# Optimization experiments

Hardware: AMD Instinct MI355X
Metric: run time of the kernel (lower is better)

The kernel has to match this reference:

```python
import jax, jax.numpy as jnp
import numpy as np

ALPHA = 0.02
NEG = -9e15

def lrelu(x):
    return jnp.where(x >= 0, x, ALPHA * x)

def layer_norm(x, eps=1e-5):
    m = jnp.mean(x, axis=-1, keepdims=True)
    v = jnp.var(x, axis=-1, keepdims=True)
    return (x - m) * jax.lax.rsqrt(v + eps)

def setup_inputs() -> dict:
    key = jax.random.key(0)
    ks = jax.random.split(key, 10)
    B, N, F_IN, D = 8, 2048, 10, 128
    h = jax.random.normal(ks[0], (B, N, F_IN), jnp.float32)
    adj = jax.random.randint(ks[1], (B, N, N), 0, 2, jnp.int32)
    s = 0.1
    return {
        "h": h,
        "adj": adj,
        "W1": jax.random.normal(ks[2], (D, F_IN), jnp.float32) * s,
        "b1": jax.random.normal(ks[3], (D,), jnp.float32) * s,
        "Wg": jax.random.normal(ks[4], (D, D), jnp.float32) * s,
        "bg": jax.random.normal(ks[5], (D,), jnp.float32) * s,
        "a1": jax.random.normal(ks[6], (D,), jnp.float32) * s,
        "a2": jax.random.normal(ks[7], (D,), jnp.float32) * s,
        "W2": jax.random.normal(ks[8], (2, D), jnp.float32) * s,
        "b2": jax.random.normal(ks[9], (2,), jnp.float32) * s,
    }

def reference(h, adj, W1, b1, Wg, bg, a1, a2, W2, b2):
    # fc1 + layernorm + leakyrelu
    x = h @ W1.T + b1                      # [B,N,128]
    x = lrelu(layer_norm(x))
    # GAT layer
    Wh = x @ Wg.T + bg                     # [B,N,128]
    e1 = Wh @ a1                           # [B,N]
    e2 = Wh @ a2                           # [B,N]
    e = lrelu(e1[:, :, None] + e2[:, None, :])  # [B,N,N]
    e = jnp.where(adj != 0, e, NEG)
    attn = jax.nn.softmax(e, axis=2)
    hp = jnp.einsum('bij,bjd->bid', attn, Wh)    # [B,N,128]
    hp = lrelu(layer_norm(hp))
    # global max pool over nodes
    pooled = jnp.max(hp, axis=1)           # [B,128]
    out = pooled @ W2.T + b2               # [B,2]
    return jax.nn.log_softmax(out, axis=-1)
```

## Files before the change

kernel.cpp:

```cpp
#include <hip/hip_runtime.h>

#define B 8
#define N 2048
#define FIN 10
#define D 128
#define ALPHA 0.02f
#define BR 32
#define TI 32
#define JC 128

typedef short bf8 __attribute__((ext_vector_type(8)));
typedef short s4v __attribute__((ext_vector_type(4)));
typedef float f32x4 __attribute__((ext_vector_type(4)));

__device__ __forceinline__ float lrelu(float x) { return x >= 0.f ? x : ALPHA * x; }

__device__ __forceinline__ short f2b(float f) {
    unsigned u = __float_as_uint(f);
    return (short)((u + 0x7fffu + ((u >> 16) & 1u)) >> 16);
}
__device__ __forceinline__ float b2f(short s) {
    return __uint_as_float(((unsigned)(unsigned short)s) << 16);
}

__device__ __forceinline__ unsigned enc_key(float v) {
    unsigned b = __float_as_uint(v);
    return (b & 0x80000000u) ? ~b : (b | 0x80000000u);
}
__device__ __forceinline__ float dec_key(unsigned k) {
    unsigned b = (k & 0x80000000u) ? (k & 0x7fffffffu) : ~k;
    return __uint_as_float(b);
}

__global__ __launch_bounds__(256) void k_proj(
    const float* __restrict__ h, const float* __restrict__ W1, const float* __restrict__ b1,
    const float* __restrict__ Wg, const float* __restrict__ bg,
    const float* __restrict__ a1, const float* __restrict__ a2,
    unsigned short* __restrict__ WhT, float* __restrict__ e1g, float* __restrict__ e2g)
{
    __shared__ __align__(16) short xep_lds[32 * 136];
    __shared__ __align__(16) short wg_lds[D * 136];
    __shared__ float W1_lds[D * 11];
    __shared__ float h_lds[BR * FIN];
    __shared__ float ep1[2][BR], ep2[2][BR];

    const int t = threadIdx.x;
    const int r0 = blockIdx.x * BR;
    const int bb = r0 >> 11;
    const int jloc = r0 & (N - 1);

    for (int idx = t; idx < D * FIN; idx += 256)
        W1_lds[(idx / FIN) * 11 + (idx % FIN)] = W1[idx];
    for (int idx = t; idx < BR * FIN; idx += 256)
        h_lds[idx] = h[(size_t)r0 * FIN + idx];
    __syncthreads();

    {
        const int dr = t >> 4;
        const int j8 = t & 15;
        #pragma unroll
        for (int pass = 0; pass < 8; pass++) {
            int dd = pass * 16 + dr;
            float4 f0 = *(const float4*)&Wg[dd * D + j8 * 8];
            float4 f1 = *(const float4*)&Wg[dd * D + j8 * 8 + 4];
            bf8 v;
            v[0] = f2b(f0.x); v[1] = f2b(f0.y); v[2] = f2b(f0.z); v[3] = f2b(f0.w);
            v[4] = f2b(f1.x); v[5] = f2b(f1.y); v[6] = f2b(f1.z); v[7] = f2b(f1.w);
            *(bf8*)&wg_lds[dd * 136 + j8 * 8] = v;
        }
    }

    const int w = t >> 6, lane = t & 63;
    {
        float b1v0 = b1[lane], b1v1 = b1[lane + 64];
        for (int i = 0; i < 8; i++) {
            int r = w * 8 + i;
            float s0 = b1v0, s1 = b1v1;
            const float* hr = &h_lds[r * FIN];
            #pragma unroll
            for (int k = 0; k < FIN; k++) {
                float hv = hr[k];
                s0 += hv * W1_lds[lane * 11 + k];
                s1 += hv * W1_lds[(lane + 64) * 11 + k];
            }
            float sm = s0 + s1, sq = s0 * s0 + s1 * s1;
            #pragma unroll
            for (int m = 1; m <= 32; m <<= 1) { sm += __shfl_xor(sm, m); sq += __shfl_xor(sq, m); }
            float mean = sm * (1.f / D);
            float var  = sq * (1.f / D) - mean * mean;
            float rs = rsqrtf(var + 1e-5f);
            xep_lds[r * 136 + lane]      = f2b(lrelu((s0 - mean) * rs));
            xep_lds[r * 136 + lane + 64] = f2b(lrelu((s1 - mean) * rs));
        }
    }
    __syncthreads();

    const int l15 = lane & 15, q = lane >> 4;
    const int mw = w & 1, np = w >> 1;
    f32x4 acc[4];
    #pragma unroll
    for (int nt = 0; nt < 4; nt++)
        #pragma unroll
        for (int r = 0; r < 4; r++) acc[nt][r] = 0.f;

    #pragma unroll
    for (int ks = 0; ks < 4; ks++) {
        bf8 av = *(const bf8*)&xep_lds[(mw * 16 + l15) * 136 + ks * 32 + q * 8];
        #pragma unroll
        for (int nt = 0; nt < 4; nt++) {
            bf8 bv = *(const bf8*)&wg_lds[((np * 4 + nt) * 16 + l15) * 136 + ks * 32 + q * 8];
            acc[nt] = __builtin_amdgcn_mfma_f32_16x16x32_bf16(av, bv, acc[nt], 0, 0, 0);
        }
    }

    float e1p[4] = {0.f, 0.f, 0.f, 0.f}, e2p[4] = {0.f, 0.f, 0.f, 0.f};
    #pragma unroll
    for (int nt = 0; nt < 4; nt++) {
        int col = (np * 4 + nt) * 16 + l15;
        float bgv = bg[col], a1v = a1[col], a2v = a2[col];
        #pragma unroll
        for (int r = 0; r < 4; r++) {
            float v = acc[nt][r] + bgv;
            acc[nt][r] = v;
            e1p[r] += v * a1v;
            e2p[r] += v * a2v;
        }
    }
    #pragma unroll
    for (int m = 1; m <= 8; m <<= 1) {
        #pragma unroll
        for (int r = 0; r < 4; r++) { e1p[r] += __shfl_xor(e1p[r], m); e2p[r] += __shfl_xor(e2p[r], m); }
    }
    if (l15 == 0) {
        #pragma unroll
        for (int r = 0; r < 4; r++) {
            ep1[np][mw * 16 + q * 4 + r] = e1p[r];
            ep2[np][mw * 16 + q * 4 + r] = e2p[r];
        }
    }
    __syncthreads();
    if (t < BR) {
        e1g[r0 + t] = ep1[0][t] + ep1[1][t];
        e2g[r0 + t] = ep2[0][t] + ep2[1][t];
    }
    #pragma unroll
    for (int nt = 0; nt < 4; nt++) {
        int col = (np * 4 + nt) * 16 + l15;
        #pragma unroll
        for (int r = 0; r < 4; r++)
            xep_lds[col * 36 + mw * 16 + q * 4 + r] = f2b(acc[nt][r]);
    }
    __syncthreads();
    {
        const int col = t >> 1, jh = (t & 1) * 16;
        unsigned short* dst = WhT + ((size_t)(bb * D + col)) * N + jloc + jh;
        #pragma unroll
        for (int i2 = 0; i2 < 4; i2++)
            *(uint2*)(dst + i2 * 4) = *(const uint2*)&xep_lds[col * 36 + jh + i2 * 4];
    }
}

__global__ __launch_bounds__(256) void k_attn(
    const int* __restrict__ adj, const unsigned short* __restrict__ WhT,
    const float* __restrict__ e1g, const float* __restrict__ e2g,
    unsigned* __restrict__ pooled)
{
    __shared__ __align__(16) short pT[TI * 136];
    __shared__ __align__(16) short whT[D * 136];
    __shared__ float e1_lds[TI];
    __shared__ float l_lds[TI];
    __shared__ float statsp[2][TI][2];
    __shared__ float maxb[2][D];

    const int t = threadIdx.x;
    const int b = blockIdx.y;
    const int i0 = blockIdx.x * TI;

    if (t < TI) { e1_lds[t] = e1g[b * N + i0 + t]; l_lds[t] = 0.f; }

    const int w = t >> 6, lane = t & 63;
    const int l15 = lane & 15, q = lane >> 4;
    const int mw = w & 1, np = w >> 1;

    const int dr = t >> 4, j8 = t & 15;
    const int jq = (t & 31) * 4, rg = t >> 5;

    const unsigned short* WhTb = WhT + (size_t)b * D * N;

    f32x4 acc[4];
    #pragma unroll
    for (int nt = 0; nt < 4; nt++)
        #pragma unroll
        for (int r = 0; r < 4; r++) acc[nt][r] = 0.f;

    for (int jc = 0; jc < N / JC; jc++) {
        const int j0 = jc * JC;
        __syncthreads();

        #pragma unroll
        for (int pass = 0; pass < 8; pass++) {
            int dd = pass * 16 + dr;
            *(bf8*)&whT[dd * 136 + j8 * 8] = *(const bf8*)(WhTb + (size_t)dd * N + j0 + j8 * 8);
        }
        {
            float4 e2v4 = *(const float4*)&e2g[b * N + j0 + jq];
            const int* ap = adj + ((size_t)b * N + i0 + rg * 4) * N + j0 + jq;
            #pragma unroll
            for (int rr = 0; rr < 4; rr++) {
                int ii = rg * 4 + rr;
                int4 a4 = *(const int4*)(ap + rr * N);
                float e1v = e1_lds[ii];
                short p0 = f2b(a4.x ? __expf(lrelu(e1v + e2v4.x)) : 0.f);
                short p1 = f2b(a4.y ? __expf(lrelu(e1v + e2v4.y)) : 0.f);
                short p2 = f2b(a4.z ? __expf(lrelu(e1v + e2v4.z)) : 0.f);
                short p3 = f2b(a4.w ? __expf(lrelu(e1v + e2v4.w)) : 0.f);
                s4v pv; pv[0] = p0; pv[1] = p1; pv[2] = p2; pv[3] = p3;
                *(s4v*)&pT[ii * 136 + jq] = pv;
                float sr = b2f(p0) + b2f(p1) + b2f(p2) + b2f(p3);
                #pragma unroll
                for (int m = 1; m <= 16; m <<= 1) sr += __shfl_xor(sr, m);
                if ((t & 31) == 0) l_lds[ii] += sr;
            }
        }
        __syncthreads();

        #pragma unroll
        for (int ks = 0; ks < 4; ks++) {
            bf8 av = *(const bf8*)&pT[(mw * 16 + l15) * 136 + ks * 32 + q * 8];
            #pragma unroll
            for (int nt = 0; nt < 4; nt++) {
                bf8 bv = *(const bf8*)&whT[((np * 4 + nt) * 16 + l15) * 136 + ks * 32 + q * 8];
                acc[nt] = __builtin_amdgcn_mfma_f32_16x16x32_bf16(av, bv, acc[nt], 0, 0, 0);
            }
        }
    }
    __syncthreads();

    float lr[4];
    #pragma unroll
    for (int r = 0; r < 4; r++) lr[r] = l_lds[mw * 16 + q * 4 + r];

    float smr[4] = {0.f, 0.f, 0.f, 0.f}, sqr[4] = {0.f, 0.f, 0.f, 0.f};
    #pragma unroll
    for (int nt = 0; nt < 4; nt++)
        #pragma unroll
        for (int r = 0; r < 4; r++) {
            float v = acc[nt][r] / lr[r];
            acc[nt][r] = v;
            smr[r] += v;
            sqr[r] += v * v;
        }
    #pragma unroll
    for (int m = 1; m <= 8; m <<= 1) {
        #pragma unroll
        for (int r = 0; r < 4; r++) { smr[r] += __shfl_xor(smr[r], m); sqr[r] += __shfl_xor(sqr[r], m); }
    }
    if (l15 == 0) {
        #pragma unroll
        for (int r = 0; r < 4; r++) {
            statsp[np][mw * 16 + q * 4 + r][0] = smr[r];
            statsp[np][mw * 16 + q * 4 + r][1] = sqr[r];
        }
    }
    __syncthreads();

    float mx[4] = {-1e30f, -1e30f, -1e30f, -1e30f};
    #pragma unroll
    for (int r = 0; r < 4; r++) {
        int row = mw * 16 + q * 4 + r;
        float s0 = statsp[0][row][0] + statsp[1][row][0];
        float s1 = statsp[0][row][1] + statsp[1][row][1];
        float mean = s0 * (1.f / D);
        float var  = s1 * (1.f / D) - mean * mean;
        float rs = rsqrtf(var + 1e-5f);
        #pragma unroll
        for (int nt = 0; nt < 4; nt++) {
            float v = lrelu((acc[nt][r] - mean) * rs);
            mx[nt] = fmaxf(mx[nt], v);
        }
    }
    #pragma unroll
    for (int m = 16; m <= 32; m <<= 1) {
        #pragma unroll
        for (int nt = 0; nt < 4; nt++) mx[nt] = fmaxf(mx[nt], __shfl_xor(mx[nt], m));
    }
    if (q == 0) {
        #pragma unroll
        for (int nt = 0; nt < 4; nt++) maxb[mw][np * 64 + nt * 16 + l15] = mx[nt];
    }
    __syncthreads();
    if (t < D) {
        float v = fmaxf(maxb[0][t], maxb[1][t]);
        atomicMax(&pooled[b * D + t], enc_key(v));
    }
}

__global__ __launch_bounds__(256) void k_final(
    const unsigned* __restrict__ pooled, const float* __restrict__ W2,
    const float* __restrict__ b2, float* __restrict__ out)
{
    const int t = threadIdx.x;
    const int b = t >> 5;
    const int q = t & 31;
    float s0 = 0.f, s1 = 0.f;
    #pragma unroll
    for (int m = 0; m < 4; m++) {
        int dd = q + 32 * m;
        float v = dec_key(pooled[b * D + dd]);
        s0 += v * W2[dd];
        s1 += v * W2[D + dd];
    }
    #pragma unroll
    for (int m = 1; m <= 16; m <<= 1) { s0 += __shfl_xor(s0, m); s1 += __shfl_xor(s1, m); }
    if (q == 0) {
        float o0 = s0 + b2[0], o1 = s1 + b2[1];
        float mxv = fmaxf(o0, o1);
        float ls = logf(__expf(o0 - mxv) + __expf(o1 - mxv));
        out[b * 2 + 0] = o0 - mxv - ls;
        out[b * 2 + 1] = o1 - mxv - ls;
    }
}

extern "C" void kernel_launch(void* const* d_in, const int* in_sizes, int n_in,
                              void* d_out, int out_size, void* d_ws, size_t ws_size,
                              hipStream_t stream) {
    const float* h   = (const float*)d_in[0];
    const int*   adj = (const int*)d_in[1];
    const float* W1  = (const float*)d_in[2];
    const float* b1  = (const float*)d_in[3];
    const float* Wg  = (const float*)d_in[4];
    const float* bg  = (const float*)d_in[5];
    const float* a1  = (const float*)d_in[6];
    const float* a2  = (const float*)d_in[7];
    const float* W2  = (const float*)d_in[8];
    const float* b2  = (const float*)d_in[9];
    float* out = (float*)d_out;

    unsigned short* WhT = (unsigned short*)d_ws;
    float* e1g = (float*)((char*)d_ws + (size_t)B * D * N * 2);
    float* e2g = e1g + (size_t)B * N;
    unsigned* pooled = (unsigned*)(e2g + (size_t)B * N);

    hipMemsetAsync(pooled, 0, B * D * sizeof(unsigned), stream);

    k_proj<<<(B * N) / BR, 256, 0, stream>>>(h, W1, b1, Wg, bg, a1, a2, WhT, e1g, e2g);
    k_attn<<<dim3(N / TI, B), 256, 0, stream>>>(adj, WhT, e1g, e2g, pooled);
    k_final<<<1, 256, 0, stream>>>(pooled, W2, b2, out);
}
```

Baseline: 252.8 us.

## Prefetch attention tiles into registers, compute row sums via MFMA, fold final kernel

The attention kernel moves to 512 threads, with each wave covering two output column tiles. It prefetches the next chunk of adj, e2 and WhT into registers while the MFMAs for the current chunk run, which removes one barrier per iteration. The softmax row sums are now an extra MFMA against a ones vector, replacing the shuffle reductions and LDS accumulation. The memset and the final kernel are folded in: k_proj clears the pooled buffer and the last attention block, found through an atomic counter, computes the output. In exchange, the denominator now sums the bf16-rounded probabilities, and correctness depends on the counter and memory fences being right.

```diff
diff --git a/kernel.cpp b/kernel.cpp
--- a/kernel.cpp
+++ b/kernel.cpp
@@ -8,6 +8,7 @@
 #define BR 32
 #define TI 32
 #define JC 128
+#define NBLK_ATTN ((N / TI) * B)
 
 typedef short bf8 __attribute__((ext_vector_type(8)));
 typedef short s4v __attribute__((ext_vector_type(4)));
@@ -18,9 +19,6 @@
 __device__ __forceinline__ short f2b(float f) {
     unsigned u = __float_as_uint(f);
     return (short)((u + 0x7fffu + ((u >> 16) & 1u)) >> 16);
-}
-__device__ __forceinline__ float b2f(short s) {
-    return __uint_as_float(((unsigned)(unsigned short)s) << 16);
 }
 
 __device__ __forceinline__ unsigned enc_key(float v) {
@@ -36,7 +34,8 @@
     const float* __restrict__ h, const float* __restrict__ W1, const float* __restrict__ b1,
     const float* __restrict__ Wg, const float* __restrict__ bg,
     const float* __restrict__ a1, const float* __restrict__ a2,
-    unsigned short* __restrict__ WhT, float* __restrict__ e1g, float* __restrict__ e2g)
+    unsigned short* __restrict__ WhT, float* __restrict__ e1g, float* __restrict__ e2g,
+    unsigned* __restrict__ pooled, unsigned* __restrict__ cnt)
 {
     __shared__ __align__(16) short xep_lds[32 * 136];
     __shared__ __align__(16) short wg_lds[D * 136];
@@ -48,6 +47,9 @@
     const int r0 = blockIdx.x * BR;
     const int bb = r0 >> 11;
     const int jloc = r0 & (N - 1);
+
+    if (blockIdx.x < B && t < D) pooled[blockIdx.x * D + t] = 0u;
+    if (blockIdx.x == 0 && t == 128) *cnt = 0u;
 
     for (int idx = t; idx < D * FIN; idx += 256)
         W1_lds[(idx / FIN) * 11 + (idx % FIN)] = W1[idx];
@@ -160,96 +162,115 @@
     }
 }
 
-__global__ __launch_bounds__(256) void k_attn(
+__global__ __launch_bounds__(512) void k_attn(
     const int* __restrict__ adj, const unsigned short* __restrict__ WhT,
     const float* __restrict__ e1g, const float* __restrict__ e2g,
-    unsigned* __restrict__ pooled)
+    unsigned* __restrict__ pooled, unsigned* __restrict__ cnt,
+    const float* __restrict__ W2, const float* __restrict__ b2,
+    float* __restrict__ out)
 {
     __shared__ __align__(16) short pT[TI * 136];
     __shared__ __align__(16) short whT[D * 136];
-    __shared__ float e1_lds[TI];
-    __shared__ float l_lds[TI];
-    __shared__ float statsp[2][TI][2];
+    __shared__ float statsp[4][TI][2];
     __shared__ float maxb[2][D];
+    __shared__ int finalflag;
 
     const int t = threadIdx.x;
     const int b = blockIdx.y;
     const int i0 = blockIdx.x * TI;
 
-    if (t < TI) { e1_lds[t] = e1g[b * N + i0 + t]; l_lds[t] = 0.f; }
-
     const int w = t >> 6, lane = t & 63;
     const int l15 = lane & 15, q = lane >> 4;
-    const int mw = w & 1, np = w >> 1;
-
-    const int dr = t >> 4, j8 = t & 15;
-    const int jq = (t & 31) * 4, rg = t >> 5;
+    const int mw = w & 1;
+    const int np = w >> 1;
+
+    const int rg = t >> 5;
+    const int jq = (t & 31) * 4;
+    const int dr = t >> 4;
+    const int j8 = t & 15;
+
+    const float e1r0 = e1g[b * N + i0 + rg * 2];
+    const float e1r1 = e1g[b * N + i0 + rg * 2 + 1];
 
     const unsigned short* WhTb = WhT + (size_t)b * D * N;
-
-    f32x4 acc[4];
-    #pragma unroll
-    for (int nt = 0; nt < 4; nt++)
+    const int* adjb = adj + ((size_t)b * N + i0) * N;
+
+    f32x4 acc[2], accl;
+    #pragma unroll
+    for (int nt = 0; nt < 2; nt++)
         #pragma unroll
         for (int r = 0; r < 4; r++) acc[nt][r] = 0.f;
+    #pragma unroll
+    for (int r = 0; r < 4; r++) accl[r] = 0.f;
+
+    bf8 ones;
+    #pragma unroll
+    for (int i = 0; i < 8; i++) ones[i] = (short)0x3F80;
+
+    int4 a0 = *(const int4*)(adjb + (size_t)(rg * 2) * N + jq);
+    int4 a1r = *(const int4*)(adjb + (size_t)(rg * 2 + 1) * N + jq);
+    float4 e2r = *(const float4*)&e2g[b * N + jq];
+    bf8 wr0 = *(const bf8*)(WhTb + (size_t)(0 * 32 + dr) * N + j8 * 8);
+    bf8 wr1 = *(const bf8*)(WhTb + (size_t)(1 * 32 + dr) * N + j8 * 8);
+    bf8 wr2 = *(const bf8*)(WhTb + (size_t)(2 * 32 + dr) * N + j8 * 8);
+    bf8 wr3 = *(const bf8*)(WhTb + (size_t)(3 * 32 + dr) * N + j8 * 8);
 
     for (int jc = 0; jc < N / JC; jc++) {
-        const int j0 = jc * JC;
+        {
+            s4v pv;
+            pv[0] = f2b(a0.x ? __expf(lrelu(e1r0 + e2r.x)) : 0.f);
+            pv[1] = f2b(a0.y ? __expf(lrelu(e1r0 + e2r.y)) : 0.f);
+            pv[2] = f2b(a0.z ? __expf(lrelu(e1r0 + e2r.z)) : 0.f);
+            pv[3] = f2b(a0.w ? __expf(lrelu(e1r0 + e2r.w)) : 0.f);
+            *(s4v*)&pT[(rg * 2) * 136 + jq] = pv;
+            pv[0] = f2b(a1r.x ? __expf(lrelu(e1r1 + e2r.x)) : 0.f);
+            pv[1] = f2b(a1r.y ? __expf(lrelu(e1r1 + e2r.y)) : 0.f);
+            pv[2] = f2b(a1r.z ? __expf(lrelu(e1r1 + e2r.z)) : 0.f);
+            pv[3] = f2b(a1r.w ? __expf(lrelu(e1r1 + e2r.w)) : 0.f);
+            *(s4v*)&pT[(rg * 2 + 1) * 136 + jq] = pv;
+            *(bf8*)&whT[(0 * 32 + dr) * 136 + j8 * 8] = wr0;
+            *(bf8*)&whT[(1 * 32 + dr) * 136 + j8 * 8] = wr1;
+            *(bf8*)&whT[(2 * 32 + dr) * 136 + j8 * 8] = wr2;
+            *(bf8*)&whT[(3 * 32 + dr) * 136 + j8 * 8] = wr3;
+        }
         __syncthreads();
 
-        #pragma unroll
-        for (int pass = 0; pass < 8; pass++) {
-            int dd = pass * 16 + dr;
-            *(bf8*)&whT[dd * 136 + j8 * 8] = *(const bf8*)(WhTb + (size_t)dd * N + j0 + j8 * 8);
-        }
-        {
-            float4 e2v4 = *(const float4*)&e2g[b * N + j0 + jq];
-            const int* ap = adj + ((size_t)b * N + i0 + rg * 4) * N + j0 + jq;
-            #pragma unroll
-            for (int rr = 0; rr < 4; rr++) {
-                int ii = rg * 4 + rr;
-                int4 a4 = *(const int4*)(ap + rr * N);
-                float e1v = e1_lds[ii];
-                short p0 = f2b(a4.x ? __expf(lrelu(e1v + e2v4.x)) : 0.f);
-                short p1 = f2b(a4.y ? __expf(lrelu(e1v + e2v4.y)) : 0.f);
-                short p2 = f2b(a4.z ? __expf(lrelu(e1v + e2v4.z)) : 0.f);
-                short p3 = f2b(a4.w ? __expf(lrelu(e1v + e2v4.w)) : 0.f);
-                s4v pv; pv[0] = p0; pv[1] = p1; pv[2] = p2; pv[3] = p3;
-                *(s4v*)&pT[ii * 136 + jq] = pv;
-                float sr = b2f(p0) + b2f(p1) + b2f(p2) + b2f(p3);
-                #pragma unroll
-                for (int m = 1; m <= 16; m <<= 1) sr += __shfl_xor(sr, m);
-                if ((t & 31) == 0) l_lds[ii] += sr;
-            }
-        }
-        __syncthreads();
+        if (jc < N / JC - 1) {
+            const int j0n = (jc + 1) * JC;
+            a0  = *(const int4*)(adjb + (size_t)(rg * 2) * N + j0n + jq);
+            a1r = *(const int4*)(adjb + (size_t)(rg * 2 + 1) * N + j0n + jq);
+            e2r = *(const float4*)&e2g[b * N + j0n + jq];
+            wr0 = *(const bf8*)(WhTb + (size_t)(0 * 32 + dr) * N + j0n + j8 * 8);
+            wr1 = *(const bf8*)(WhTb + (size_t)(1 * 32 + dr) * N + j0n + j8 * 8);
+            wr2 = *(const bf8*)(WhTb + (size_t)(2 * 32 + dr) * N + j0n + j8 * 8);
+            wr3 = *(const bf8*)(WhTb + (size_t)(3 * 32 + dr) * N + j0n + j8 * 8);
+        }
 
         #pragma unroll
         for (int ks = 0; ks < 4; ks++) {
             bf8 av = *(const bf8*)&pT[(mw * 16 + l15) * 136 + ks * 32 + q * 8];
             #pragma unroll
-            for (int nt = 0; nt < 4; nt++) {
-                bf8 bv = *(const bf8*)&whT[((np * 4 + nt) * 16 + l15) * 136 + ks * 32 + q * 8];
+            for (int nt = 0; nt < 2; nt++) {
+                bf8 bv = *(const bf8*)&whT[((np * 2 + nt) * 16 + l15) * 136 + ks * 32 + q * 8];
                 acc[nt] = __builtin_amdgcn_mfma_f32_16x16x32_bf16(av, bv, acc[nt], 0, 0, 0);
             }
-        }
-    }
-    __syncthreads();
-
-    float lr[4];
-    #pragma unroll
-    for (int r = 0; r < 4; r++) lr[r] = l_lds[mw * 16 + q * 4 + r];
+            accl = __builtin_amdgcn_mfma_f32_16x16x32_bf16(av, ones, accl, 0, 0, 0);
+        }
+        __syncthreads();
+    }
 
     float smr[4] = {0.f, 0.f, 0.f, 0.f}, sqr[4] = {0.f, 0.f, 0.f, 0.f};
     #pragma unroll
-    for (int nt = 0; nt < 4; nt++)
-        #pragma unroll
-        for (int r = 0; r < 4; r++) {
-            float v = acc[nt][r] / lr[r];
+    for (int r = 0; r < 4; r++) {
+        float rinv = 1.f / accl[r];
+        #pragma unroll
+        for (int nt = 0; nt < 2; nt++) {
+            float v = acc[nt][r] * rinv;
             acc[nt][r] = v;
             smr[r] += v;
             sqr[r] += v * v;
         }
+    }
     #pragma unroll
     for (int m = 1; m <= 8; m <<= 1) {
         #pragma unroll
@@ -264,17 +285,17 @@
     }
     __syncthreads();
 
-    float mx[4] = {-1e30f, -1e30f, -1e30f, -1e30f};
+    float mx[2] = {-1e30f, -1e30f};
     #pragma unroll
     for (int r = 0; r < 4; r++) {
         int row = mw * 16 + q * 4 + r;
-        float s0 = statsp[0][row][0] + statsp[1][row][0];
-        float s1 = statsp[0][row][1] + statsp[1][row][1];
+        float s0 = statsp[0][row][0] + statsp[1][row][0] + statsp[2][row][0] + statsp[3][row][0];
+        float s1 = statsp[0][row][1] + statsp[1][row][1] + statsp[2][row][1] + statsp[3][row][1];
         float mean = s0 * (1.f / D);
         float var  = s1 * (1.f / D) - mean * mean;
         float rs = rsqrtf(var + 1e-5f);
         #pragma unroll
-        for (int nt = 0; nt < 4; nt++) {
+        for (int nt = 0; nt < 2; nt++) {
             float v = lrelu((acc[nt][r] - mean) * rs);
             mx[nt] = fmaxf(mx[nt], v);
         }
@@ -282,42 +303,47 @@
     #pragma unroll
     for (int m = 16; m <= 32; m <<= 1) {
         #pragma unroll
-        for (int nt = 0; nt < 4; nt++) mx[nt] = fmaxf(mx[nt], __shfl_xor(mx[nt], m));
+        for (int nt = 0; nt < 2; nt++) mx[nt] = fmaxf(mx[nt], __shfl_xor(mx[nt], m));
     }
     if (q == 0) {
         #pragma unroll
-        for (int nt = 0; nt < 4; nt++) maxb[mw][np * 64 + nt * 16 + l15] = mx[nt];
+        for (int nt = 0; nt < 2; nt++) maxb[mw][(np * 2 + nt) * 16 + l15] = mx[nt];
     }
     __syncthreads();
     if (t < D) {
         float v = fmaxf(maxb[0][t], maxb[1][t]);
         atomicMax(&pooled[b * D + t], enc_key(v));
     }
-}
-
-__global__ __launch_bounds__(256) void k_final(
-    const unsigned* __restrict__ pooled, const float* __restrict__ W2,
-    const float* __restrict__ b2, float* __restrict__ out)
-{
-    const int t = threadIdx.x;
-    const int b = t >> 5;
-    const int q = t & 31;
-    float s0 = 0.f, s1 = 0.f;
-    #pragma unroll
-    for (int m = 0; m < 4; m++) {
-        int dd = q + 32 * m;
-        float v = dec_key(pooled[b * D + dd]);
-        s0 += v * W2[dd];
-        s1 += v * W2[D + dd];
-    }
-    #pragma unroll
-    for (int m = 1; m <= 16; m <<= 1) { s0 += __shfl_xor(s0, m); s1 += __shfl_xor(s1, m); }
-    if (q == 0) {
-        float o0 = s0 + b2[0], o1 = s1 + b2[1];
-        float mxv = fmaxf(o0, o1);
-        float ls = logf(__expf(o0 - mxv) + __expf(o1 - mxv));
-        out[b * 2 + 0] = o0 - mxv - ls;
-        out[b * 2 + 1] = o1 - mxv - ls;
+    __syncthreads();
+
+    if (t == 0) {
+        __threadfence();
+        unsigned old = atomicAdd(cnt, 1u);
+        finalflag = (old == NBLK_ATTN - 1) ? 1 : 0;
+    }
+    __syncthreads();
+    if (finalflag && t < 256) {
+        const int fb = t >> 5;
+        const int fq = t & 31;
+        float s0 = 0.f, s1 = 0.f;
+        #pragma unroll
+        for (int m = 0; m < 4; m++) {
+            int dd = fq + 32 * m;
+            unsigned key = __hip_atomic_load(&pooled[fb * D + dd], __ATOMIC_RELAXED,
+                                             __HIP_MEMORY_SCOPE_AGENT);
+            float v = dec_key(key);
+            s0 += v * W2[dd];
+            s1 += v * W2[D + dd];
+        }
+        #pragma unroll
+        for (int m = 1; m <= 16; m <<= 1) { s0 += __shfl_xor(s0, m); s1 += __shfl_xor(s1, m); }
+        if (fq == 0) {
+            float o0 = s0 + b2[0], o1 = s1 + b2[1];
+            float mxv = fmaxf(o0, o1);
+            float ls = logf(__expf(o0 - mxv) + __expf(o1 - mxv));
+            out[fb * 2 + 0] = o0 - mxv - ls;
+            out[fb * 2 + 1] = o1 - mxv - ls;
+        }
     }
 }
 
@@ -340,10 +366,10 @@
     float* e1g = (float*)((char*)d_ws + (size_t)B * D * N * 2);
     float* e2g = e1g + (size_t)B * N;
     unsigned* pooled = (unsigned*)(e2g + (size_t)B * N);
-
-    hipMemsetAsync(pooled, 0, B * D * sizeof(unsigned), stream);
-
-    k_proj<<<(B * N) / BR, 256, 0, stream>>>(h, W1, b1, Wg, bg, a1, a2, WhT, e1g, e2g);
-    k_attn<<<dim3(N / TI, B), 256, 0, stream>>>(adj, WhT, e1g, e2g, pooled);
-    k_final<<<1, 256, 0, stream>>>(pooled, W2, b2, out);
-}
+    unsigned* cnt = pooled + (size_t)B * D;
+
+    k_proj<<<(B * N) / BR, 256, 0, stream>>>(h, W1, b1, Wg, bg, a1, a2,
+                                             WhT, e1g, e2g, pooled, cnt);
+    k_attn<<<dim3(N / TI, B), 512, 0, stream>>>(adj, WhT, e1g, e2g, pooled, cnt,
+                                                W2, b2, out);
+}
```

Measured after the change: 238.4 us. 5.7% less time.
